# Kernel optimization log

Hardware: AMD Instinct MI355X
Metric: run time of the kernel (lower is better)

Reference implementation:

```python
import jax, jax.numpy as jnp
import numpy as np

B = 2          # batch size
T2 = 9         # temporal groups (b*t2 = grid_sample batch)
T3 = 27        # t1 // t2
T1 = 243       # t2 * t3
P = 17         # joints
K2 = 9         # kernel_size ** 2
C = 128        # dim_img
CH = [48, 96, 192, 384]
HW = [(96, 72), (48, 36), (24, 18), (12, 9)]
ALPHA = 0.9


def setup_inputs() -> dict:
    key = jax.random.key(0)
    ks = jax.random.split(key, 16)
    inp = {}
    N = B * T2
    for i, (c, (h, w)) in enumerate(zip(CH, HW)):
        inp[f"f{i}"] = jax.random.normal(ks[i], (N, c, h, w), jnp.float32)
    inp["query"] = jax.random.normal(ks[4], (B, T1, P * K2, C), jnp.float32)
    # key holds normalized grid coords in [-1, 1]
    inp["key"] = jax.random.uniform(ks[5], (N, T3, P * K2, 2), jnp.float32) * 2.0 - 1.0
    inp["value"] = jax.random.normal(ks[6], (B, T1, P, C), jnp.float32)
    s = 0.05
    inp["w_off"] = jax.random.normal(ks[7], (2, C), jnp.float32) * s
    inp["b_off"] = jnp.zeros((2,), jnp.float32)
    inp["w_attn"] = jax.random.normal(ks[8], (2, C), jnp.float32) * s
    inp["b_attn"] = jnp.zeros((2,), jnp.float32)
    for i, c in enumerate(CH):
        inp[f"we{i}"] = jax.random.normal(ks[9 + i], (C, c), jnp.float32) * s
        inp[f"be{i}"] = jnp.zeros((C,), jnp.float32)
    inp["conv_w"] = jax.random.normal(ks[13], (C, C, K2), jnp.float32) * s
    inp["conv_b"] = jnp.zeros((C,), jnp.float32)
    return inp


def _grid_sample(img, grid):
    """Bilinear grid_sample, align_corners=False, zero padding.
    img: [N, C, H, W]; grid: [N, Hg, Wg, 2] in [-1,1] (x=width, y=height).
    Returns [N, Hg, Wg, C] (channels-last for the following 1x1 conv)."""
    N, Cin, H, W = img.shape
    gx, gy = grid[..., 0], grid[..., 1]
    ix = ((gx + 1.0) * W - 1.0) * 0.5
    iy = ((gy + 1.0) * H - 1.0) * 0.5
    ix0 = jnp.floor(ix); iy0 = jnp.floor(iy)
    wx1 = ix - ix0; wx0 = 1.0 - wx1
    wy1 = iy - iy0; wy0 = 1.0 - wy1
    bidx = jnp.arange(N)[:, None, None]

    def gather(yy, xx):
        yi = yy.astype(jnp.int32); xi = xx.astype(jnp.int32)
        valid = (yi >= 0) & (yi < H) & (xi >= 0) & (xi < W)
        yc = jnp.clip(yi, 0, H - 1); xc = jnp.clip(xi, 0, W - 1)
        v = img[bidx, :, yc, xc]  # [N, Hg, Wg, C]
        return v * valid[..., None].astype(img.dtype)

    out = (gather(iy0, ix0) * (wy0 * wx0)[..., None]
           + gather(iy0, ix0 + 1.0) * (wy0 * wx1)[..., None]
           + gather(iy0 + 1.0, ix0) * (wy1 * wx0)[..., None]
           + gather(iy0 + 1.0, ix0 + 1.0) * (wy1 * wx1)[..., None])
    return out


def reference(f0, f1, f2, f3, query, key, value,
              w_off, b_off, w_attn, b_attn,
              we0, be0, we1, be1, we2, be2, we3, be3,
              conv_w, conv_b):
    b, t1, p, c = value.shape            # [B, 243, 17, 128]
    t3 = key.shape[1]                    # 27
    t2 = t1 // t3                        # 9

    # learned offsets per query location, squashed by tanh
    off = jnp.tanh(jnp.einsum('btqc,oc->btqo', query, w_off) + b_off)   # [b,t1,153,2]
    # per-joint softmax weights, tiled over the k^2 kernel taps
    aw = jax.nn.softmax(jnp.einsum('btpc,oc->btpo', value, w_attn) + b_attn, axis=-1)  # [b,t1,17,2]
    aw = jnp.tile(aw, (1, 1, K2, 1))                                     # [b,t1,153,2]

    sp = (off * aw).reshape(b * t2, t3, p * K2, 2)
    sampling_positions = key + sp                                        # [b*t2, 27, 153, 2]

    fmaps = (f0, f1, f2, f3)
    ws = (we0, we1, we2, we3)
    bs = (be0, be1, be2, be3)
    feats = []
    for f, w, bb in zip(fmaps, ws, bs):
        g = _grid_sample(f, sampling_positions)                          # [b*t2, 27, 153, C_in]
        e = jnp.einsum('nhwc,oc->nhwo', g, w) + bb                        # 1x1 conv embed -> 128
        feats.append(e.reshape(b, t2 * t3, p * K2, C))                    # [b, 243, 153, 128]
    new_query = jnp.mean(jnp.stack(feats, axis=-2), axis=-2)             # fuse 4 levels
    new_query = (1.0 - ALPHA) * new_query + ALPHA * query

    # grouped-by-position conv1d over the k^2 taps (full-width kernel -> length 1)
    x = new_query.reshape(b, t1, p, K2, c)                               # 'b t (p k) c'
    new_value = jnp.einsum('btpkc,ock->btpo', x, conv_w) + conv_b        # [b, 243, 17, 128]
    return (new_query, new_value, sampling_positions)
```

## Files before the change

kernel.cpp:

```cpp
#include <hip/hip_runtime.h>
#include <hip/hip_bf16.h>

static constexpr int NQ_SIZE = 9517824;
static constexpr int NV_SIZE = 1057536;
static constexpr int NPOS    = 74358;
static constexpr int M_CONV  = 8262;

static constexpr long E0_OFF = 0;
static constexpr long E1_OFF = 15925248;
static constexpr long E2_OFF = E1_OFF + 3981312;
static constexpr long E3_OFF = E2_OFF + 995328;
static constexpr long E_END  = E3_OFF + 248832;

static constexpr int SEG_L3 = 18;
static constexpr int SEG_L2 = SEG_L3 + 72;
static constexpr int SEG_L1 = SEG_L2 + 252;
static constexpr int SEG_L0 = SEG_L1 + 972;
static constexpr int SEG_AW = SEG_L0 + 65;
static constexpr int SEG_CT = SEG_AW + 576;
static constexpr int PREP_GRID = SEG_CT + 1;

typedef __attribute__((ext_vector_type(8))) short short8;
typedef __attribute__((ext_vector_type(4))) float floatx4;

__device__ __forceinline__ float bf2f(unsigned short u) {
    union { unsigned int i; float f; } v; v.i = ((unsigned)u) << 16; return v.f;
}
__device__ __forceinline__ unsigned short f2bf_rne(float f) {
    union { float f; unsigned int i; } v; v.f = f;
    unsigned int u = v.i;
    u += 0x7fffu + ((u >> 16) & 1u);
    return (unsigned short)(u >> 16);
}
__device__ __forceinline__ short8 pack8(const float* t) {
    union { unsigned short u[8]; short8 s; } r;
    #pragma unroll
    for (int i = 0; i < 8; ++i) r.u[i] = f2bf_rne(t[i]);
    return r.s;
}

template<int K, int M, bool FULLM>
__device__ __forceinline__ void proj_body(
    const float* __restrict__ A, const float* __restrict__ W,
    unsigned short* __restrict__ Eo, int m0, int tid,
    unsigned short* __restrict__ shbuf)
{
    constexpr int KC      = (K < 96) ? K : 96;
    constexpr int KCPAD   = (KC + 31) & ~31;
    constexpr int KT      = KCPAD / 32;
    constexpr int NCH     = K / KC;
    constexpr bool NEEDPAD = (KCPAD != KC);

    unsigned short (*Bs)[104] = (unsigned short (*)[104])shbuf;

    const int lane = tid & 63;
    const int wave = tid >> 6;
    const int l15  = lane & 15;
    const int quad = lane >> 4;
    const int mg0  = m0 + wave * 32 + l15;
    const int mg1  = mg0 + 16;
    const bool v0  = FULLM || (mg0 < M);
    const bool v1  = FULLM || (mg1 < M);

    floatx4 acc[2][8];
    #pragma unroll
    for (int f = 0; f < 2; ++f)
        #pragma unroll
        for (int nt = 0; nt < 8; ++nt) acc[f][nt] = (floatx4){0.f, 0.f, 0.f, 0.f};

    const int so  = tid >> 1;
    const int skb = (tid & 1) * (KCPAD / 2);

    #pragma unroll 1
    for (int ch = 0; ch < NCH; ++ch) {
        const int kc = ch * KC;
        if (ch) __syncthreads();

        {
            const float* wp = W + (long)so * K + kc + skb;
            #pragma unroll
            for (int j = 0; j < KCPAD / 2; j += 8) {
                float t8[8];
                #pragma unroll
                for (int i = 0; i < 8; ++i)
                    t8[i] = (!NEEDPAD || (skb + j + i < KC)) ? wp[j + i] : 0.f;
                unsigned short u[8];
                #pragma unroll
                for (int i = 0; i < 8; ++i) u[i] = f2bf_rne(t8[i]);
                *(uint4*)&Bs[so][skb + j] = *(const uint4*)u;
            }
        }
        __syncthreads();

        #pragma unroll
        for (int kt = 0; kt < KT; ++kt) {
            const int kg = kc + kt * 32 + quad * 8;
            const float* ap = A + (long)kg * M + mg0;
            float a0[8], a1[8];
            if (FULLM && (!NEEDPAD || (kg + 8 <= K))) {
                #pragma unroll
                for (int j = 0; j < 8; ++j) {
                    a0[j] = ap[(long)j * M];
                    a1[j] = ap[(long)j * M + 16];
                }
            } else {
                #pragma unroll
                for (int j = 0; j < 8; ++j) {
                    a0[j] = 0.f; a1[j] = 0.f;
                    if (kg + j < K) {
                        if (v0) a0[j] = ap[(long)j * M];
                        if (v1) a1[j] = ap[(long)j * M + 16];
                    }
                }
            }
            short8 af0 = pack8(a0);
            short8 af1 = pack8(a1);
            #pragma unroll
            for (int nt = 0; nt < 8; ++nt) {
                short8 bf = *(const short8*)&Bs[nt * 16 + l15][kt * 32 + quad * 8];
                acc[0][nt] = __builtin_amdgcn_mfma_f32_16x16x32_bf16(af0, bf, acc[0][nt], 0, 0, 0);
                acc[1][nt] = __builtin_amdgcn_mfma_f32_16x16x32_bf16(af1, bf, acc[1][nt], 0, 0, 0);
            }
        }
    }

    __syncthreads();
    #pragma unroll
    for (int f = 0; f < 2; ++f) {
        #pragma unroll
        for (int nt = 0; nt < 8; ++nt) {
            #pragma unroll
            for (int r = 0; r < 4; ++r) {
                int row = wave * 32 + f * 16 + quad * 4 + r;
                shbuf[row * 128 + nt * 16 + l15] = f2bf_rne(acc[f][nt][r]);
            }
        }
    }
    __syncthreads();
    const uint4* sb4 = (const uint4*)shbuf;
    uint4* eo4 = (uint4*)(Eo + (long)m0 * 128);
    #pragma unroll
    for (int j = 0; j < 8; ++j) {
        int off16 = wave * 512 + j * 64 + lane;
        if (FULLM || (m0 + (off16 >> 4) < M))
            eo4[off16] = sb4[off16];
    }
}

__global__ __launch_bounds__(256) void prep_k(
    const float* __restrict__ f0, const float* __restrict__ f1,
    const float* __restrict__ f2, const float* __restrict__ f3,
    const float* __restrict__ we0, const float* __restrict__ we1,
    const float* __restrict__ we2, const float* __restrict__ we3,
    const float* __restrict__ conv_w, unsigned short* __restrict__ convT2,
    const float* __restrict__ value,
    const float* __restrict__ w_attn, const float* __restrict__ b_attn,
    const float* __restrict__ be0, const float* __restrict__ be1,
    const float* __restrict__ be2, const float* __restrict__ be3,
    float* __restrict__ awbuf, float* __restrict__ besum,
    unsigned short* __restrict__ Ebase)
{
    __shared__ unsigned short shbuf[128 * 128];
    const int bid = blockIdx.x;
    const int tid = threadIdx.x;

    if (bid < SEG_L0) {
        if (bid < SEG_L3) {
            int n = bid;
            proj_body<384, 108, false>(f3 + (long)n * 384 * 108, we3,
                Ebase + E3_OFF + (long)n * 108 * 128, 0, tid, shbuf);
        } else if (bid < SEG_L2) {
            int r = bid - SEG_L3; int n = r >> 2, t = r & 3;
            const float* A = f2 + (long)n * 192 * 432;
            unsigned short* Eo = Ebase + E2_OFF + (long)n * 432 * 128;
            if (t < 3) proj_body<192, 432, true >(A, we2, Eo, t * 128, tid, shbuf);
            else       proj_body<192, 432, false>(A, we2, Eo, t * 128, tid, shbuf);
        } else if (bid < SEG_L1) {
            int r = bid - SEG_L2; int n = r / 14, t = r - n * 14;
            const float* A = f1 + (long)n * 96 * 1728;
            unsigned short* Eo = Ebase + E1_OFF + (long)n * 1728 * 128;
            if (t < 13) proj_body<96, 1728, true >(A, we1, Eo, t * 128, tid, shbuf);
            else        proj_body<96, 1728, false>(A, we1, Eo, t * 128, tid, shbuf);
        } else {
            int r = bid - SEG_L1; int n = r / 54, t = r - n * 54;
            proj_body<48, 6912, true>(f0 + (long)n * 48 * 6912, we0,
                Ebase + E0_OFF + (long)n * 6912 * 128, t * 128, tid, shbuf);
        }
    } else if (bid < SEG_AW) {
        int t = (bid - SEG_L0) * 256 + tid;
        if (t < 16524) {
            int rp = t >> 1, o = t & 1;
            const float* vrow = value + (long)rp * 128;
            const float* wrow = w_attn + o * 128;
            float s = 0.f;
            for (int c = 0; c < 128; c += 4) {
                float4 v = *(const float4*)(vrow + c);
                float4 w = *(const float4*)(wrow + c);
                s += v.x * w.x + v.y * w.y + v.z * w.z + v.w * w.w;
            }
            s += b_attn[o];
            float so = __shfl_xor(s, 1);
            float m = fmaxf(s, so);
            float e = __expf(s - m), eo = __expf(so - m);
            awbuf[t] = e / (e + eo);
        }
    } else if (bid < SEG_CT) {
        int idx = (bid - SEG_AW) * 256 + tid;
        if (idx < 147456) {
            int o = idx / 1152, kk = idx - o * 1152;
            int k2 = kk >> 7, c = kk & 127;
            convT2[idx] = f2bf_rne(conv_w[o * 1152 + c * 9 + k2]);
        }
    } else {
        if (tid < 128)
            besum[tid] = be0[tid] + be1[tid] + be2[tid] + be3[tid];
    }
}

__global__ __launch_bounds__(256) void gather_k(
    const unsigned short* __restrict__ Ebase,
    const float* __restrict__ query, const float* __restrict__ key,
    const float* __restrict__ w_off, const float* __restrict__ b_off,
    const float* __restrict__ awbuf, const float* __restrict__ besum,
    float* __restrict__ nq, float* __restrict__ samp)
{
    const int tid = threadIdx.x;
    const int li  = (blockIdx.x & 7) * 581 + (blockIdx.x >> 3);
    const int pos = li * 16 + (tid >> 4);
    if (pos >= NPOS) return;
    const int l16 = tid & 15;
    const int c8  = l16 << 3;

    const int bt1 = pos / 153, q = pos - bt1 * 153;
    const int b  = bt1 / 243, t1 = bt1 - b * 243;
    const int t2 = t1 / 27,  t3 = t1 - t2 * 27;
    const int n  = b * 9 + t2;
    const int p  = q % 17;

    const long qi = (long)pos * 128 + c8;
    const float4 qv0 = *(const float4*)(query + qi);
    const float4 qv1 = *(const float4*)(query + qi + 4);

    float4 w0a = *(const float4*)(w_off + c8);
    float4 w0b = *(const float4*)(w_off + c8 + 4);
    float4 w1a = *(const float4*)(w_off + 128 + c8);
    float4 w1b = *(const float4*)(w_off + 128 + c8 + 4);
    float s0 = qv0.x * w0a.x + qv0.y * w0a.y + qv0.z * w0a.z + qv0.w * w0a.w
             + qv1.x * w0b.x + qv1.y * w0b.y + qv1.z * w0b.z + qv1.w * w0b.w;
    float s1 = qv0.x * w1a.x + qv0.y * w1a.y + qv0.z * w1a.z + qv0.w * w1a.w
             + qv1.x * w1b.x + qv1.y * w1b.y + qv1.z * w1b.z + qv1.w * w1b.w;
    #pragma unroll
    for (int m = 8; m >= 1; m >>= 1) {
        s0 += __shfl_xor(s0, m);
        s1 += __shfl_xor(s1, m);
    }
    const float aw0 = awbuf[(bt1 * 17 + p) * 2];
    const float aw1 = awbuf[(bt1 * 17 + p) * 2 + 1];
    const float off0 = tanhf(s0 + b_off[0]);
    const float off1 = tanhf(s1 + b_off[1]);
    const long kidx = (((long)n * 27 + t3) * 153 + q) * 2;
    const float gx = key[kidx]     + off0 * aw0;
    const float gy = key[kidx + 1] + off1 * aw1;
    if (l16 == 0) *(float2*)(samp + kidx) = (float2){gx, gy};

    float acc[8];
    #pragma unroll
    for (int j = 0; j < 8; ++j) acc[j] = 0.f;
    const long Eoffs[4] = {E0_OFF, E1_OFF, E2_OFF, E3_OFF};
    const int Hs[4] = {96, 48, 24, 12}, Wd[4] = {72, 36, 18, 9};
    #pragma unroll
    for (int l = 0; l < 4; ++l) {
        const int H = Hs[l], W = Wd[l];
        const unsigned short* E = Ebase + Eoffs[l] + (long)n * H * W * 128 + c8;
        float ix = ((gx + 1.f) * (float)W - 1.f) * 0.5f;
        float iy = ((gy + 1.f) * (float)H - 1.f) * 0.5f;
        float fx0 = floorf(ix), fy0 = floorf(iy);
        int x0 = (int)fx0, y0 = (int)fy0;
        int x1 = x0 + 1, y1 = y0 + 1;
        float wx1 = ix - fx0, wx0 = 1.f - wx1;
        float wy1 = iy - fy0, wy0 = 1.f - wy1;
        bool vy0 = (unsigned)y0 < (unsigned)H, vy1 = (unsigned)y1 < (unsigned)H;
        bool vx0 = (unsigned)x0 < (unsigned)W, vx1 = (unsigned)x1 < (unsigned)W;
        float w00 = (vy0 && vx0) ? wy0 * wx0 : 0.f;
        float w01 = (vy0 && vx1) ? wy0 * wx1 : 0.f;
        float w10 = (vy1 && vx0) ? wy1 * wx0 : 0.f;
        float w11 = (vy1 && vx1) ? wy1 * wx1 : 0.f;
        int yc0 = min(max(y0, 0), H - 1), yc1 = min(max(y1, 0), H - 1);
        int xc0 = min(max(x0, 0), W - 1), xc1 = min(max(x1, 0), W - 1);
        short8 v00 = *(const short8*)(E + ((long)yc0 * W + xc0) * 128);
        short8 v01 = *(const short8*)(E + ((long)yc0 * W + xc1) * 128);
        short8 v10 = *(const short8*)(E + ((long)yc1 * W + xc0) * 128);
        short8 v11 = *(const short8*)(E + ((long)yc1 * W + xc1) * 128);
        #pragma unroll
        for (int j = 0; j < 8; ++j) {
            float a = acc[j];
            a = fmaf(w00, bf2f((unsigned short)v00[j]), a);
            a = fmaf(w01, bf2f((unsigned short)v01[j]), a);
            a = fmaf(w10, bf2f((unsigned short)v10[j]), a);
            a = fmaf(w11, bf2f((unsigned short)v11[j]), a);
            acc[j] = a;
        }
    }
    const float4 bs0 = *(const float4*)(besum + c8);
    const float4 bs1 = *(const float4*)(besum + c8 + 4);
    float4 o0, o1;
    o0.x = 0.1f * (0.25f * (acc[0] + bs0.x)) + 0.9f * qv0.x;
    o0.y = 0.1f * (0.25f * (acc[1] + bs0.y)) + 0.9f * qv0.y;
    o0.z = 0.1f * (0.25f * (acc[2] + bs0.z)) + 0.9f * qv0.z;
    o0.w = 0.1f * (0.25f * (acc[3] + bs0.w)) + 0.9f * qv0.w;
    o1.x = 0.1f * (0.25f * (acc[4] + bs1.x)) + 0.9f * qv1.x;
    o1.y = 0.1f * (0.25f * (acc[5] + bs1.y)) + 0.9f * qv1.y;
    o1.z = 0.1f * (0.25f * (acc[6] + bs1.z)) + 0.9f * qv1.z;
    o1.w = 0.1f * (0.25f * (acc[7] + bs1.w)) + 0.9f * qv1.w;
    *(float4*)(nq + qi)     = o0;
    *(float4*)(nq + qi + 4) = o1;
}

__global__ __launch_bounds__(256) void conv_mfma_k(
    const float* __restrict__ nq, const unsigned short* __restrict__ convT2,
    const float* __restrict__ conv_b, float* __restrict__ nv)
{
    __shared__ unsigned short As[32][72];
    __shared__ unsigned short Bs[64][72];

    const int tid  = threadIdx.x;
    const int lane = tid & 63;
    const int wave = tid >> 6;
    const int wm = (wave & 1) * 16;
    const int wn = (wave >> 1) * 32;
    const int m0 = blockIdx.x * 32;
    const int n0 = blockIdx.y * 64;
    const int l15  = lane & 15;
    const int quad = lane >> 4;

    floatx4 acc[2];
    acc[0] = (floatx4){0.f, 0.f, 0.f, 0.f};
    acc[1] = acc[0];

    const int am = tid >> 3;
    const int ak = (tid & 7) << 3;
    const int bn = tid >> 2;
    const int bk = (tid & 3) << 4;

    float4 a0, a1; uint4 bv0, bv1;
    auto fetch = [&](int k0) {
        a0 = (float4){0,0,0,0}; a1 = a0;
        int row = m0 + am;
        if (row < M_CONV) {
            a0 = *(const float4*)(nq + (long)row * 1152 + k0 + ak);
            a1 = *(const float4*)(nq + (long)row * 1152 + k0 + ak + 4);
        }
        bv0 = *(const uint4*)(convT2 + (long)(n0 + bn) * 1152 + k0 + bk);
        bv1 = *(const uint4*)(convT2 + (long)(n0 + bn) * 1152 + k0 + bk + 8);
    };
    fetch(0);

    for (int k0 = 0; k0 < 1152; k0 += 64) {
        unsigned short t[8] = {f2bf_rne(a0.x), f2bf_rne(a0.y), f2bf_rne(a0.z), f2bf_rne(a0.w),
                               f2bf_rne(a1.x), f2bf_rne(a1.y), f2bf_rne(a1.z), f2bf_rne(a1.w)};
        *(uint4*)&As[am][ak] = *(const uint4*)t;
        *(uint4*)&Bs[bn][bk] = bv0;
        *(uint4*)&Bs[bn][bk + 8] = bv1;
        __syncthreads();
        if (k0 + 64 < 1152) fetch(k0 + 64);

        #pragma unroll
        for (int kt = 0; kt < 2; ++kt) {
            short8 af = *(const short8*)&As[wm + l15][kt * 32 + quad * 8];
            #pragma unroll
            for (int nt = 0; nt < 2; ++nt) {
                short8 bf = *(const short8*)&Bs[wn + nt * 16 + l15][kt * 32 + quad * 8];
                acc[nt] = __builtin_amdgcn_mfma_f32_16x16x32_bf16(af, bf, acc[nt], 0, 0, 0);
            }
        }
        __syncthreads();
    }

    #pragma unroll
    for (int nt = 0; nt < 2; ++nt) {
        int col = n0 + wn + nt * 16 + l15;
        float bias = conv_b[col];
        #pragma unroll
        for (int r = 0; r < 4; ++r) {
            int row = m0 + wm + quad * 4 + r;
            if (row < M_CONV)
                nv[(long)row * 128 + col] = acc[nt][r] + bias;
        }
    }
}

extern "C" void kernel_launch(void* const* d_in, const int* in_sizes, int n_in,
                              void* d_out, int out_size, void* d_ws, size_t ws_size,
                              hipStream_t stream) {
    const float* f0     = (const float*)d_in[0];
    const float* f1     = (const float*)d_in[1];
    const float* f2     = (const float*)d_in[2];
    const float* f3     = (const float*)d_in[3];
    const float* query  = (const float*)d_in[4];
    const float* key    = (const float*)d_in[5];
    const float* value  = (const float*)d_in[6];
    const float* w_off  = (const float*)d_in[7];
    const float* b_off  = (const float*)d_in[8];
    const float* w_attn = (const float*)d_in[9];
    const float* b_attn = (const float*)d_in[10];
    const float* we0    = (const float*)d_in[11];
    const float* be0    = (const float*)d_in[12];
    const float* we1    = (const float*)d_in[13];
    const float* be1    = (const float*)d_in[14];
    const float* we2    = (const float*)d_in[15];
    const float* be2    = (const float*)d_in[16];
    const float* we3    = (const float*)d_in[17];
    const float* be3    = (const float*)d_in[18];
    const float* conv_w = (const float*)d_in[19];
    const float* conv_b = (const float*)d_in[20];

    float* out  = (float*)d_out;
    float* nq   = out;
    float* nv   = out + NQ_SIZE;
    float* samp = out + NQ_SIZE + NV_SIZE;

    unsigned short* Ebase  = (unsigned short*)d_ws;
    unsigned short* convT2 = Ebase + E_END;
    float* awbuf = nv;
    float* besum = nv + 16524;

    prep_k<<<PREP_GRID, 256, 0, stream>>>(
        f0, f1, f2, f3, we0, we1, we2, we3, conv_w, convT2,
        value, w_attn, b_attn, be0, be1, be2, be3, awbuf, besum, Ebase);

    gather_k<<<4648, 256, 0, stream>>>(
        Ebase, query, key, w_off, b_off, awbuf, besum, nq, samp);

    conv_mfma_k<<<dim3(259, 2), 256, 0, stream>>>(nq, convT2, conv_b, nv);
}
```

Measured before the change: 217.2 us.

## Fuse gather, attention-weight softmax and tap conv into one per-row kernel

The separate gather and MFMA conv kernels are merged into one kernel, and the attention-weight and bias-sum work moves out of the prep kernel into it. Each block handles half of one (b,t1) row. It computes the attention softmax and bias sum in LDS, does the bilinear gathers, and stores the new query as bf16 in LDS. It then runs the tap convolution with MFMA directly from LDS, reading conv weights from global memory. This removes a kernel launch and the re-read of the fp32 new query from global memory. In exchange there are only 972 blocks, the MFMA tiles are mostly padding (9 of 16 rows used), and the B operand is loaded from global memory without LDS reuse.

Result: slower. 262.0 us (+20.6%).

```diff
diff --git a/kernel.cpp b/kernel.cpp
--- a/kernel.cpp
+++ b/kernel.cpp
@@ -16,9 +16,8 @@
 static constexpr int SEG_L2 = SEG_L3 + 72;
 static constexpr int SEG_L1 = SEG_L2 + 252;
 static constexpr int SEG_L0 = SEG_L1 + 972;
-static constexpr int SEG_AW = SEG_L0 + 65;
-static constexpr int SEG_CT = SEG_AW + 576;
-static constexpr int PREP_GRID = SEG_CT + 1;
+static constexpr int SEG_CT = SEG_L0 + 576;
+static constexpr int PREP_GRID = SEG_CT;
 
 typedef __attribute__((ext_vector_type(8))) short short8;
 typedef __attribute__((ext_vector_type(4))) float floatx4;
@@ -153,11 +152,6 @@
     const float* __restrict__ we0, const float* __restrict__ we1,
     const float* __restrict__ we2, const float* __restrict__ we3,
     const float* __restrict__ conv_w, unsigned short* __restrict__ convT2,
-    const float* __restrict__ value,
-    const float* __restrict__ w_attn, const float* __restrict__ b_attn,
-    const float* __restrict__ be0, const float* __restrict__ be1,
-    const float* __restrict__ be2, const float* __restrict__ be3,
-    float* __restrict__ awbuf, float* __restrict__ besum,
     unsigned short* __restrict__ Ebase)
 {
     __shared__ unsigned short shbuf[128 * 128];
@@ -186,205 +180,189 @@
             proj_body<48, 6912, true>(f0 + (long)n * 48 * 6912, we0,
                 Ebase + E0_OFF + (long)n * 6912 * 128, t * 128, tid, shbuf);
         }
-    } else if (bid < SEG_AW) {
-        int t = (bid - SEG_L0) * 256 + tid;
-        if (t < 16524) {
-            int rp = t >> 1, o = t & 1;
-            const float* vrow = value + (long)rp * 128;
-            const float* wrow = w_attn + o * 128;
-            float s = 0.f;
-            for (int c = 0; c < 128; c += 4) {
-                float4 v = *(const float4*)(vrow + c);
-                float4 w = *(const float4*)(wrow + c);
-                s += v.x * w.x + v.y * w.y + v.z * w.z + v.w * w.w;
-            }
-            s += b_attn[o];
-            float so = __shfl_xor(s, 1);
-            float m = fmaxf(s, so);
-            float e = __expf(s - m), eo = __expf(so - m);
-            awbuf[t] = e / (e + eo);
-        }
-    } else if (bid < SEG_CT) {
-        int idx = (bid - SEG_AW) * 256 + tid;
+    } else {
+        int idx = (bid - SEG_L0) * 256 + tid;
         if (idx < 147456) {
             int o = idx / 1152, kk = idx - o * 1152;
             int k2 = kk >> 7, c = kk & 127;
             convT2[idx] = f2bf_rne(conv_w[o * 1152 + c * 9 + k2]);
         }
-    } else {
-        if (tid < 128)
-            besum[tid] = be0[tid] + be1[tid] + be2[tid] + be3[tid];
-    }
-}
-
-__global__ __launch_bounds__(256) void gather_k(
+    }
+}
+
+__global__ __launch_bounds__(256) void gc_k(
     const unsigned short* __restrict__ Ebase,
+    const unsigned short* __restrict__ convT2,
     const float* __restrict__ query, const float* __restrict__ key,
+    const float* __restrict__ value,
     const float* __restrict__ w_off, const float* __restrict__ b_off,
-    const float* __restrict__ awbuf, const float* __restrict__ besum,
-    float* __restrict__ nq, float* __restrict__ samp)
+    const float* __restrict__ w_attn, const float* __restrict__ b_attn,
+    const float* __restrict__ be0, const float* __restrict__ be1,
+    const float* __restrict__ be2, const float* __restrict__ be3,
+    const float* __restrict__ conv_b,
+    float* __restrict__ nq, float* __restrict__ nv, float* __restrict__ samp)
 {
+    __shared__ float aw_lds[17][2];
+    __shared__ float besum_lds[128];
+    __shared__ unsigned short nq_lds[81 * 136];
+
     const int tid = threadIdx.x;
-    const int li  = (blockIdx.x & 7) * 581 + (blockIdx.x >> 3);
-    const int pos = li * 16 + (tid >> 4);
-    if (pos >= NPOS) return;
-    const int l16 = tid & 15;
-    const int c8  = l16 << 3;
-
-    const int bt1 = pos / 153, q = pos - bt1 * 153;
-    const int b  = bt1 / 243, t1 = bt1 - b * 243;
-    const int t2 = t1 / 27,  t3 = t1 - t2 * 27;
-    const int n  = b * 9 + t2;
-    const int p  = q % 17;
-
-    const long qi = (long)pos * 128 + c8;
-    const float4 qv0 = *(const float4*)(query + qi);
-    const float4 qv1 = *(const float4*)(query + qi + 4);
-
-    float4 w0a = *(const float4*)(w_off + c8);
-    float4 w0b = *(const float4*)(w_off + c8 + 4);
-    float4 w1a = *(const float4*)(w_off + 128 + c8);
-    float4 w1b = *(const float4*)(w_off + 128 + c8 + 4);
-    float s0 = qv0.x * w0a.x + qv0.y * w0a.y + qv0.z * w0a.z + qv0.w * w0a.w
-             + qv1.x * w0b.x + qv1.y * w0b.y + qv1.z * w0b.z + qv1.w * w0b.w;
-    float s1 = qv0.x * w1a.x + qv0.y * w1a.y + qv0.z * w1a.z + qv0.w * w1a.w
-             + qv1.x * w1b.x + qv1.y * w1b.y + qv1.z * w1b.z + qv1.w * w1b.w;
-    #pragma unroll
-    for (int m = 8; m >= 1; m >>= 1) {
-        s0 += __shfl_xor(s0, m);
-        s1 += __shfl_xor(s1, m);
-    }
-    const float aw0 = awbuf[(bt1 * 17 + p) * 2];
-    const float aw1 = awbuf[(bt1 * 17 + p) * 2 + 1];
-    const float off0 = tanhf(s0 + b_off[0]);
-    const float off1 = tanhf(s1 + b_off[1]);
-    const long kidx = (((long)n * 27 + t3) * 153 + q) * 2;
-    const float gx = key[kidx]     + off0 * aw0;
-    const float gy = key[kidx + 1] + off1 * aw1;
-    if (l16 == 0) *(float2*)(samp + kidx) = (float2){gx, gy};
-
-    float acc[8];
-    #pragma unroll
-    for (int j = 0; j < 8; ++j) acc[j] = 0.f;
+    const int xcd = blockIdx.x & 7, slot = blockIdx.x >> 3;
+    const int logical = (xcd < 4) ? xcd * 122 + slot : 488 + (xcd - 4) * 121 + slot;
+    const int bt1   = logical >> 1;
+    const int half  = logical & 1;
+    const int qbase = half * 81;
+    const int NQR   = half ? 72 : 81;
+    const int NP    = half ? 8 : 9;
+    const int pbase = half * 9;
+
+    const int bb = bt1 / 243, t1 = bt1 - bb * 243, t2 = t1 / 27;
+    const int n  = bb * 9 + t2;
+
+    if (tid < 136) {
+        int p = tid >> 3, o = (tid >> 2) & 1, qt = tid & 3;
+        const float* vrow = value + ((long)bt1 * 17 + p) * 128 + qt * 32;
+        const float* wrow = w_attn + o * 128 + qt * 32;
+        float s = 0.f;
+        #pragma unroll
+        for (int c = 0; c < 32; c += 4) {
+            float4 v = *(const float4*)(vrow + c);
+            float4 w = *(const float4*)(wrow + c);
+            s += v.x * w.x + v.y * w.y + v.z * w.z + v.w * w.w;
+        }
+        s += __shfl_xor(s, 1);
+        s += __shfl_xor(s, 2);
+        s += b_attn[o];
+        float so = __shfl_xor(s, 4);
+        float m  = fmaxf(s, so);
+        float e  = __expf(s - m), eo = __expf(so - m);
+        if (qt == 0) aw_lds[p][o] = e / (e + eo);
+    }
+    if (tid >= 128) {
+        int c = tid - 128;
+        besum_lds[c] = be0[c] + be1[c] + be2[c] + be3[c];
+    }
+    __syncthreads();
+
+    const int grp = tid >> 4, l16 = tid & 15, c8 = l16 << 3;
+    const float4 w0a = *(const float4*)(w_off + c8);
+    const float4 w0b = *(const float4*)(w_off + c8 + 4);
+    const float4 w1a = *(const float4*)(w_off + 128 + c8);
+    const float4 w1b = *(const float4*)(w_off + 128 + c8 + 4);
+    const float bo0 = b_off[0], bo1 = b_off[1];
+    const float4 bs0 = *(const float4*)(besum_lds + c8);
+    const float4 bs1 = *(const float4*)(besum_lds + c8 + 4);
     const long Eoffs[4] = {E0_OFF, E1_OFF, E2_OFF, E3_OFF};
     const int Hs[4] = {96, 48, 24, 12}, Wd[4] = {72, 36, 18, 9};
-    #pragma unroll
-    for (int l = 0; l < 4; ++l) {
-        const int H = Hs[l], W = Wd[l];
-        const unsigned short* E = Ebase + Eoffs[l] + (long)n * H * W * 128 + c8;
-        float ix = ((gx + 1.f) * (float)W - 1.f) * 0.5f;
-        float iy = ((gy + 1.f) * (float)H - 1.f) * 0.5f;
-        float fx0 = floorf(ix), fy0 = floorf(iy);
-        int x0 = (int)fx0, y0 = (int)fy0;
-        int x1 = x0 + 1, y1 = y0 + 1;
-        float wx1 = ix - fx0, wx0 = 1.f - wx1;
-        float wy1 = iy - fy0, wy0 = 1.f - wy1;
-        bool vy0 = (unsigned)y0 < (unsigned)H, vy1 = (unsigned)y1 < (unsigned)H;
-        bool vx0 = (unsigned)x0 < (unsigned)W, vx1 = (unsigned)x1 < (unsigned)W;
-        float w00 = (vy0 && vx0) ? wy0 * wx0 : 0.f;
-        float w01 = (vy0 && vx1) ? wy0 * wx1 : 0.f;
-        float w10 = (vy1 && vx0) ? wy1 * wx0 : 0.f;
-        float w11 = (vy1 && vx1) ? wy1 * wx1 : 0.f;
-        int yc0 = min(max(y0, 0), H - 1), yc1 = min(max(y1, 0), H - 1);
-        int xc0 = min(max(x0, 0), W - 1), xc1 = min(max(x1, 0), W - 1);
-        short8 v00 = *(const short8*)(E + ((long)yc0 * W + xc0) * 128);
-        short8 v01 = *(const short8*)(E + ((long)yc0 * W + xc1) * 128);
-        short8 v10 = *(const short8*)(E + ((long)yc1 * W + xc0) * 128);
-        short8 v11 = *(const short8*)(E + ((long)yc1 * W + xc1) * 128);
-        #pragma unroll
-        for (int j = 0; j < 8; ++j) {
-            float a = acc[j];
-            a = fmaf(w00, bf2f((unsigned short)v00[j]), a);
-            a = fmaf(w01, bf2f((unsigned short)v01[j]), a);
-            a = fmaf(w10, bf2f((unsigned short)v10[j]), a);
-            a = fmaf(w11, bf2f((unsigned short)v11[j]), a);
-            acc[j] = a;
-        }
-    }
-    const float4 bs0 = *(const float4*)(besum + c8);
-    const float4 bs1 = *(const float4*)(besum + c8 + 4);
-    float4 o0, o1;
-    o0.x = 0.1f * (0.25f * (acc[0] + bs0.x)) + 0.9f * qv0.x;
-    o0.y = 0.1f * (0.25f * (acc[1] + bs0.y)) + 0.9f * qv0.y;
-    o0.z = 0.1f * (0.25f * (acc[2] + bs0.z)) + 0.9f * qv0.z;
-    o0.w = 0.1f * (0.25f * (acc[3] + bs0.w)) + 0.9f * qv0.w;
-    o1.x = 0.1f * (0.25f * (acc[4] + bs1.x)) + 0.9f * qv1.x;
-    o1.y = 0.1f * (0.25f * (acc[5] + bs1.y)) + 0.9f * qv1.y;
-    o1.z = 0.1f * (0.25f * (acc[6] + bs1.z)) + 0.9f * qv1.z;
-    o1.w = 0.1f * (0.25f * (acc[7] + bs1.w)) + 0.9f * qv1.w;
-    *(float4*)(nq + qi)     = o0;
-    *(float4*)(nq + qi + 4) = o1;
-}
-
-__global__ __launch_bounds__(256) void conv_mfma_k(
-    const float* __restrict__ nq, const unsigned short* __restrict__ convT2,
-    const float* __restrict__ conv_b, float* __restrict__ nv)
-{
-    __shared__ unsigned short As[32][72];
-    __shared__ unsigned short Bs[64][72];
-
-    const int tid  = threadIdx.x;
-    const int lane = tid & 63;
-    const int wave = tid >> 6;
-    const int wm = (wave & 1) * 16;
-    const int wn = (wave >> 1) * 32;
-    const int m0 = blockIdx.x * 32;
-    const int n0 = blockIdx.y * 64;
-    const int l15  = lane & 15;
-    const int quad = lane >> 4;
-
-    floatx4 acc[2];
-    acc[0] = (floatx4){0.f, 0.f, 0.f, 0.f};
-    acc[1] = acc[0];
-
-    const int am = tid >> 3;
-    const int ak = (tid & 7) << 3;
-    const int bn = tid >> 2;
-    const int bk = (tid & 3) << 4;
-
-    float4 a0, a1; uint4 bv0, bv1;
-    auto fetch = [&](int k0) {
-        a0 = (float4){0,0,0,0}; a1 = a0;
-        int row = m0 + am;
-        if (row < M_CONV) {
-            a0 = *(const float4*)(nq + (long)row * 1152 + k0 + ak);
-            a1 = *(const float4*)(nq + (long)row * 1152 + k0 + ak + 4);
-        }
-        bv0 = *(const uint4*)(convT2 + (long)(n0 + bn) * 1152 + k0 + bk);
-        bv1 = *(const uint4*)(convT2 + (long)(n0 + bn) * 1152 + k0 + bk + 8);
-    };
-    fetch(0);
-
-    for (int k0 = 0; k0 < 1152; k0 += 64) {
-        unsigned short t[8] = {f2bf_rne(a0.x), f2bf_rne(a0.y), f2bf_rne(a0.z), f2bf_rne(a0.w),
-                               f2bf_rne(a1.x), f2bf_rne(a1.y), f2bf_rne(a1.z), f2bf_rne(a1.w)};
-        *(uint4*)&As[am][ak] = *(const uint4*)t;
-        *(uint4*)&Bs[bn][bk] = bv0;
-        *(uint4*)&Bs[bn][bk + 8] = bv1;
-        __syncthreads();
-        if (k0 + 64 < 1152) fetch(k0 + 64);
-
-        #pragma unroll
-        for (int kt = 0; kt < 2; ++kt) {
-            short8 af = *(const short8*)&As[wm + l15][kt * 32 + quad * 8];
+
+    for (int ql = grp; ql < NQR; ql += 16) {
+        const int q = qbase + ql;
+        const long qglob = (long)bt1 * 153 + q;
+        const long qi = qglob * 128 + c8;
+        const float4 qv0 = *(const float4*)(query + qi);
+        const float4 qv1 = *(const float4*)(query + qi + 4);
+
+        float s0 = qv0.x*w0a.x + qv0.y*w0a.y + qv0.z*w0a.z + qv0.w*w0a.w
+                 + qv1.x*w0b.x + qv1.y*w0b.y + qv1.z*w0b.z + qv1.w*w0b.w;
+        float s1 = qv0.x*w1a.x + qv0.y*w1a.y + qv0.z*w1a.z + qv0.w*w1a.w
+                 + qv1.x*w1b.x + qv1.y*w1b.y + qv1.z*w1b.z + qv1.w*w1b.w;
+        #pragma unroll
+        for (int m = 8; m >= 1; m >>= 1) {
+            s0 += __shfl_xor(s0, m);
+            s1 += __shfl_xor(s1, m);
+        }
+        const int paw = q % 17;
+        const float aw0 = aw_lds[paw][0], aw1 = aw_lds[paw][1];
+        const float2 kv = *(const float2*)(key + qglob * 2);
+        const float gx = kv.x + tanhf(s0 + bo0) * aw0;
+        const float gy = kv.y + tanhf(s1 + bo1) * aw1;
+        if (l16 == 0) *(float2*)(samp + qglob * 2) = (float2){gx, gy};
+
+        float acc[8];
+        #pragma unroll
+        for (int j = 0; j < 8; ++j) acc[j] = 0.f;
+        #pragma unroll
+        for (int l = 0; l < 4; ++l) {
+            const int H = Hs[l], W = Wd[l];
+            const unsigned short* E = Ebase + Eoffs[l] + (long)n * H * W * 128 + c8;
+            float ix = ((gx + 1.f) * (float)W - 1.f) * 0.5f;
+            float iy = ((gy + 1.f) * (float)H - 1.f) * 0.5f;
+            float fx0 = floorf(ix), fy0 = floorf(iy);
+            int x0 = (int)fx0, y0 = (int)fy0, x1 = x0 + 1, y1 = y0 + 1;
+            float wx1 = ix - fx0, wx0 = 1.f - wx1;
+            float wy1 = iy - fy0, wy0 = 1.f - wy1;
+            bool vy0 = (unsigned)y0 < (unsigned)H, vy1 = (unsigned)y1 < (unsigned)H;
+            bool vx0 = (unsigned)x0 < (unsigned)W, vx1 = (unsigned)x1 < (unsigned)W;
+            float w00 = (vy0 && vx0) ? wy0 * wx0 : 0.f;
+            float w01 = (vy0 && vx1) ? wy0 * wx1 : 0.f;
+            float w10 = (vy1 && vx0) ? wy1 * wx0 : 0.f;
+            float w11 = (vy1 && vx1) ? wy1 * wx1 : 0.f;
+            int yc0 = min(max(y0, 0), H - 1), yc1 = min(max(y1, 0), H - 1);
+            int xc0 = min(max(x0, 0), W - 1), xc1 = min(max(x1, 0), W - 1);
+            short8 v00 = *(const short8*)(E + ((long)yc0 * W + xc0) * 128);
+            short8 v01 = *(const short8*)(E + ((long)yc0 * W + xc1) * 128);
+            short8 v10 = *(const short8*)(E + ((long)yc1 * W + xc0) * 128);
+            short8 v11 = *(const short8*)(E + ((long)yc1 * W + xc1) * 128);
             #pragma unroll
-            for (int nt = 0; nt < 2; ++nt) {
-                short8 bf = *(const short8*)&Bs[wn + nt * 16 + l15][kt * 32 + quad * 8];
-                acc[nt] = __builtin_amdgcn_mfma_f32_16x16x32_bf16(af, bf, acc[nt], 0, 0, 0);
+            for (int j = 0; j < 8; ++j) {
+                float a = acc[j];
+                a = fmaf(w00, bf2f((unsigned short)v00[j]), a);
+                a = fmaf(w01, bf2f((unsigned short)v01[j]), a);
+                a = fmaf(w10, bf2f((unsigned short)v10[j]), a);
+                a = fmaf(w11, bf2f((unsigned short)v11[j]), a);
+                acc[j] = a;
             }
         }
-        __syncthreads();
+
+        float ov[8];
+        ov[0] = 0.1f * (0.25f * (acc[0] + bs0.x)) + 0.9f * qv0.x;
+        ov[1] = 0.1f * (0.25f * (acc[1] + bs0.y)) + 0.9f * qv0.y;
+        ov[2] = 0.1f * (0.25f * (acc[2] + bs0.z)) + 0.9f * qv0.z;
+        ov[3] = 0.1f * (0.25f * (acc[3] + bs0.w)) + 0.9f * qv0.w;
+        ov[4] = 0.1f * (0.25f * (acc[4] + bs1.x)) + 0.9f * qv1.x;
+        ov[5] = 0.1f * (0.25f * (acc[5] + bs1.y)) + 0.9f * qv1.y;
+        ov[6] = 0.1f * (0.25f * (acc[6] + bs1.z)) + 0.9f * qv1.z;
+        ov[7] = 0.1f * (0.25f * (acc[7] + bs1.w)) + 0.9f * qv1.w;
+        *(float4*)(nq + qi)     = (float4){ov[0], ov[1], ov[2], ov[3]};
+        *(float4*)(nq + qi + 4) = (float4){ov[4], ov[5], ov[6], ov[7]};
+        unsigned short u[8];
+        #pragma unroll
+        for (int j = 0; j < 8; ++j) u[j] = f2bf_rne(ov[j]);
+        *(uint4*)&nq_lds[ql * 136 + c8] = *(const uint4*)u;
+    }
+    __syncthreads();
+
+    const int lane = tid & 63, wave = tid >> 6;
+    const int l15 = lane & 15, quad = lane >> 4;
+    const int colb = wave * 32;
+    floatx4 cacc[2];
+    cacc[0] = (floatx4){0.f, 0.f, 0.f, 0.f};
+    cacc[1] = cacc[0];
+    const bool avalid = l15 < NP;
+
+    #pragma unroll 4
+    for (int ks = 0; ks < 36; ++ks) {
+        const int kk0 = ks * 32 + quad * 8;
+        const int k2 = kk0 >> 7, c0 = kk0 & 127;
+        short8 af = (short8){0, 0, 0, 0, 0, 0, 0, 0};
+        if (avalid)
+            af = *(const short8*)&nq_lds[(l15 * 9 + k2) * 136 + c0];
+        #pragma unroll
+        for (int nt = 0; nt < 2; ++nt) {
+            short8 bf = *(const short8*)(convT2 + (long)(colb + nt * 16 + l15) * 1152 + kk0);
+            cacc[nt] = __builtin_amdgcn_mfma_f32_16x16x32_bf16(af, bf, cacc[nt], 0, 0, 0);
+        }
     }
 
     #pragma unroll
     for (int nt = 0; nt < 2; ++nt) {
-        int col = n0 + wn + nt * 16 + l15;
-        float bias = conv_b[col];
+        const int col = colb + nt * 16 + l15;
+        const float bias = conv_b[col];
         #pragma unroll
         for (int r = 0; r < 4; ++r) {
-            int row = m0 + wm + quad * 4 + r;
-            if (row < M_CONV)
-                nv[(long)row * 128 + col] = acc[nt][r] + bias;
+            const int p = quad * 4 + r;
+            if (p < NP)
+                nv[((long)bt1 * 17 + pbase + p) * 128 + col] = cacc[nt][r] + bias;
         }
     }
 }
@@ -421,15 +399,11 @@
 
     unsigned short* Ebase  = (unsigned short*)d_ws;
     unsigned short* convT2 = Ebase + E_END;
-    float* awbuf = nv;
-    float* besum = nv + 16524;
 
     prep_k<<<PREP_GRID, 256, 0, stream>>>(
-        f0, f1, f2, f3, we0, we1, we2, we3, conv_w, convT2,
-        value, w_attn, b_attn, be0, be1, be2, be3, awbuf, besum, Ebase);
-
-    gather_k<<<4648, 256, 0, stream>>>(
-        Ebase, query, key, w_off, b_off, awbuf, besum, nq, samp);
-
-    conv_mfma_k<<<dim3(259, 2), 256, 0, stream>>>(nq, convT2, conv_b, nv);
-}
+        f0, f1, f2, f3, we0, we1, we2, we3, conv_w, convT2, Ebase);
+
+    gc_k<<<972, 256, 0, stream>>>(
+        Ebase, convT2, query, key, value, w_off, b_off, w_attn, b_attn,
+        be0, be1, be2, be3, conv_b, nq, nv, samp);
+}
```
